# Kernel tuning notes

Measured on AMD Instinct MI355X. Metric: run time of the kernel, lower is better.

The kernel has to match this reference:

```python
import jax, jax.numpy as jnp
import numpy as np

CH = 256
RED = 4
CQK = CH // RED

def _conv(x, w, b):
    # x: [B,C,H,W], w: [O,I,3,3], b: [O]; SAME padding (pad=1)
    y = jax.lax.conv_general_dilated(
        x, w, window_strides=(1, 1), padding=((1, 1), (1, 1)),
        dimension_numbers=('NCHW', 'OIHW', 'NCHW'))
    return y + b[None, :, None, None]

def setup_inputs() -> dict:
    key = jax.random.key(0)
    ks = jax.random.split(key, 7)
    x = jax.random.normal(ks[0], (4, CH, 64, 64), dtype=jnp.float32)
    fan_in = CH * 9
    s = 1.0 / np.sqrt(fan_in)
    q_w = jax.random.uniform(ks[1], (CQK, CH, 3, 3), jnp.float32, -s, s)
    q_b = jax.random.uniform(ks[2], (CQK,), jnp.float32, -s, s)
    k_w = jax.random.uniform(ks[3], (CQK, CH, 3, 3), jnp.float32, -s, s)
    k_b = jax.random.uniform(ks[4], (CQK,), jnp.float32, -s, s)
    v_w = jax.random.uniform(ks[5], (CH, CH, 3, 3), jnp.float32, -s, s)
    v_b = jax.random.uniform(ks[6], (CH,), jnp.float32, -s, s)
    return {"x": x, "q_w": q_w, "q_b": q_b, "k_w": k_w, "k_b": k_b,
            "v_w": v_w, "v_b": v_b}

def reference(x, q_w, q_b, k_w, k_b, v_w, v_b):
    b, c, h, w = x.shape
    hw = h * w
    scale = CQK ** (-0.5)
    q = _conv(x, q_w, q_b).reshape(b, CQK, hw)   # [B, Cqk, HW]
    k = _conv(x, k_w, k_b).reshape(b, CQK, hw)   # [B, Cqk, HW]
    v = _conv(x, v_w, v_b).reshape(b, c, hw)     # [B, C,   HW]
    # attn[b,i,j] = sum_d q[b,d,i] * k[b,d,j]
    attn = jnp.einsum('bdi,bdj->bij', q, k) * scale
    attn = jax.nn.softmax(attn, axis=-1)         # [B, HW, HW]
    # out[b,c,i] = sum_j v[b,c,j] * attn[b,i,j]  (torch: bmm(v, attn^T))
    out = jnp.einsum('bcj,bij->bci', v, attn).reshape(b, c, h, w)
    return out
```

## Files before the change

### kernel.cpp

```cpp
#include <hip/hip_runtime.h>
#include <stdint.h>

typedef unsigned short u16;
typedef short short8 __attribute__((ext_vector_type(8)));
typedef short short4v __attribute__((ext_vector_type(4)));
typedef float float4v __attribute__((ext_vector_type(4)));
typedef float float16v __attribute__((ext_vector_type(16)));
typedef uint32_t uint2v __attribute__((ext_vector_type(2)));

#define HW 4096
#define QSCL 0.18033688011112042f

#define GLOAD_LDS(g, l) __builtin_amdgcn_global_load_lds( \
    (const __attribute__((address_space(1))) void*)(g),   \
    (__attribute__((address_space(3))) void*)(l), 16, 0, 0)

static __device__ __forceinline__ u16 f2bf(float f) {
  union { float f; uint32_t u; } v; v.f = f;
  uint32_t r = v.u + 0x7fffu + ((v.u >> 16) & 1u);
  return (u16)(r >> 16);
}

static __device__ __forceinline__ uint32_t pkbf(float a, float b) {
  uint32_t r;
  asm("v_cvt_pk_bf16_f32 %0, %1, %2" : "=v"(r) : "v"(a), "v"(b));
  return r;
}

__global__ __launch_bounds__(256) void k_xt(const float* __restrict__ x, u16* __restrict__ Xtp) {
  __shared__ float t[32][33];
  const int b = blockIdx.z, c0 = blockIdx.y * 32, p0 = blockIdx.x * 32;
  const int tid = threadIdx.x;
  const int l8 = tid >> 5, lp = tid & 31;
#pragma unroll
  for (int i = 0; i < 4; i++) {
    int c = l8 + i * 8;
    t[c][lp] = x[(size_t)(b * 256 + c0 + c) * HW + p0 + lp];
  }
  __syncthreads();
#pragma unroll
  for (int i = 0; i < 4; i++) {
    int p = l8 + i * 8;
    int pp = p0 + p;
    int y = pp >> 6, xx = pp & 63;
    Xtp[((size_t)(b * 66 + y + 1) * 66 + (xx + 1)) * 256 + c0 + lp] = f2bf(t[lp][p]);
  }
}

__global__ __launch_bounds__(256) void k_wprep(const float* __restrict__ qw, const float* __restrict__ qb,
    const float* __restrict__ kw, const float* __restrict__ kb,
    const float* __restrict__ vw, const float* __restrict__ vb,
    u16* __restrict__ Wt, float* __restrict__ bcat) {
  int tid = blockIdx.x * 256 + threadIdx.x;
  if (tid < 9 * 384 * 256) {
    int ci = tid & 255;
    int n = (tid >> 8) % 384;
    int off = tid / (384 * 256);
    float val;
    if (n < 64)       val = qw[(size_t)n * 2304 + ci * 9 + off];
    else if (n < 128) val = kw[(size_t)(n - 64) * 2304 + ci * 9 + off];
    else              val = vw[(size_t)(n - 128) * 2304 + ci * 9 + off];
    Wt[tid] = f2bf(val);
  }
  if (tid < 384) bcat[tid] = (tid < 64) ? qb[tid] : (tid < 128) ? kb[tid - 64] : vb[tid - 128];
}

__global__ __launch_bounds__(256) void k_conv(const u16* __restrict__ Xtp,
    const u16* __restrict__ Wt, const float* __restrict__ bcat,
    u16* __restrict__ Qt, u16* __restrict__ Kt, u16* __restrict__ Vcf) {
  __shared__ __align__(16) u16 Als[2][128 * 64];
  __shared__ __align__(16) u16 Bls[2][64 * 64];
  const int tid = threadIdx.x;
  const int b = blockIdx.z, ct = blockIdx.y;
  const int p0 = blockIdx.x * 128, n0 = ct * 64;
  const int w = tid >> 6, lane = tid & 63, l16 = lane & 15, quad = lane >> 4;

  const int lr = lane >> 3, lcx = (lane & 7) ^ lr;
  const u16* ag[4];
#pragma unroll
  for (int g = 0; g < 4; g++) {
    const int pos = p0 + w * 32 + g * 8 + lr;
    const int py = pos >> 6, px = pos & 63;
    ag[g] = Xtp + ((size_t)(b * 66 + py) * 66 + px) * 256 + lcx * 8;
  }
  const u16* bg[2];
#pragma unroll
  for (int g = 0; g < 2; g++)
    bg[g] = Wt + (size_t)(n0 + w * 16 + g * 8 + lr) * 256 + lcx * 8;

  const int rx = l16 & 7;

  float4v acc[2][4];
  const float4v zz = {0.f, 0.f, 0.f, 0.f};
#pragma unroll
  for (int i = 0; i < 2; i++)
#pragma unroll
    for (int j = 0; j < 4; j++) acc[i][j] = zz;

#pragma unroll
  for (int g = 0; g < 4; g++) GLOAD_LDS(ag[g], &Als[0][(w * 32 + g * 8) * 64]);
#pragma unroll
  for (int g = 0; g < 2; g++) GLOAD_LDS(bg[g], &Bls[0][(w * 16 + g * 8) * 64]);
  __syncthreads();

  for (int ks = 0; ks < 36; ks++) {
    const int buf = ks & 1;
    if (ks + 1 < 36) {
      const int ksn = ks + 1, tap = ksn >> 2, cg = (ksn & 3) * 64;
      const int dy = (tap * 11) >> 5, dx = tap - dy * 3;
      const int aoff = (dy * 66 + dx) * 256 + cg;
      const size_t boff = (size_t)tap * 98304 + cg;
#pragma unroll
      for (int g = 0; g < 4; g++) GLOAD_LDS(ag[g] + aoff, &Als[buf ^ 1][(w * 32 + g * 8) * 64]);
#pragma unroll
      for (int g = 0; g < 2; g++) GLOAD_LDS(bg[g] + boff, &Bls[buf ^ 1][(w * 16 + g * 8) * 64]);
    }

    short8 af[2][2], bfv[4][2];
#pragma unroll
    for (int mt = 0; mt < 2; mt++)
#pragma unroll
      for (int kk = 0; kk < 2; kk++)
        af[mt][kk] = *(const short8*)&Als[buf][(w * 32 + mt * 16 + l16) * 64 + (((kk * 4 + quad) ^ rx) * 8)];
#pragma unroll
    for (int nt = 0; nt < 4; nt++)
#pragma unroll
      for (int kk = 0; kk < 2; kk++)
        bfv[nt][kk] = *(const short8*)&Bls[buf][(nt * 16 + l16) * 64 + (((kk * 4 + quad) ^ rx) * 8)];

    if (ct < 2) {
#pragma unroll
      for (int mt = 0; mt < 2; mt++)
#pragma unroll
        for (int nt = 0; nt < 4; nt++)
#pragma unroll
          for (int kk = 0; kk < 2; kk++)
            acc[mt][nt] = __builtin_amdgcn_mfma_f32_16x16x32_bf16(bfv[nt][kk], af[mt][kk], acc[mt][nt], 0, 0, 0);
    } else {
#pragma unroll
      for (int mt = 0; mt < 2; mt++)
#pragma unroll
        for (int nt = 0; nt < 4; nt++)
#pragma unroll
          for (int kk = 0; kk < 2; kk++)
            acc[mt][nt] = __builtin_amdgcn_mfma_f32_16x16x32_bf16(af[mt][kk], bfv[nt][kk], acc[mt][nt], 0, 0, 0);
    }
    __syncthreads();
  }

  if (ct < 2) {
    u16* base = (ct == 0) ? Qt : Kt;
    const float qs = (ct == 0) ? QSCL : 1.0f;
#pragma unroll
    for (int mt = 0; mt < 2; mt++) {
      const int p = p0 + w * 32 + mt * 16 + l16;
#pragma unroll
      for (int nt = 0; nt < 4; nt++) {
        const int nb = nt * 16 + quad * 4;
        short4v o;
#pragma unroll
        for (int r = 0; r < 4; r++) o[r] = (short)f2bf((acc[mt][nt][r] + bcat[ct * 64 + nb + r]) * qs);
        *(short4v*)(base + (size_t)(b * HW + p) * 64 + nb) = o;
      }
    }
  } else {
#pragma unroll
    for (int mt = 0; mt < 2; mt++) {
      const int pb = p0 + w * 32 + mt * 16 + quad * 4;
#pragma unroll
      for (int nt = 0; nt < 4; nt++) {
        const int cl = nt * 16 + l16;
        const int gc = (ct - 2) * 64 + cl;
        const float bias = bcat[ct * 64 + cl];
        short4v o;
#pragma unroll
        for (int r = 0; r < 4; r++) o[r] = (short)f2bf(acc[mt][nt][r] + bias);
        *(short4v*)(Vcf + (size_t)(b * 256 + gc) * HW + pb) = o;
      }
    }
  }
}

__global__ __launch_bounds__(512, 2) void k_attn(const u16* __restrict__ Qt,
    const u16* __restrict__ Kt, const u16* __restrict__ Vcf, float* __restrict__ out) {
  __shared__ __align__(16) u16 Kls[2][64 * 64];
  __shared__ __align__(16) u16 Vls[2][256 * 64];
  __shared__ __align__(16) u16 Pls[64 * 64];
  __shared__ float Lls[4][64];

  const int tid = threadIdx.x;
  const int b = blockIdx.y, ib = blockIdx.x * 64;
  const int w = tid >> 6, lane = tid & 63;
  const int l16 = lane & 15, quad = lane >> 4;
  const int l32 = lane & 31, half = lane >> 5;
  const int jb = w & 3, ih = w >> 2;
  const int cb = w;

  const u16* Kb = Kt + (size_t)b * HW * 64;
  const u16* Vb = Vcf + (size_t)b * 256 * HW;

  const int lr = lane >> 3, lcx = (lane & 7) ^ lr;
  const size_t koff = (size_t)(w * 8 + lr) * 128 + (size_t)lcx * 16;
  const size_t voff = (size_t)lr * (HW * 2) + (size_t)lcx * 16;

  const int krow = (jb * 16 + l16) * 64;
  const int kc0 = (quad ^ (l16 & 7)) * 8;
  const int kc1 = ((4 + quad) ^ (l16 & 7)) * 8;

  short8 qf[2][2];
  {
    const u16* qp = Qt + ((size_t)(b * HW + ib + ih * 32 + l16)) * 64 + quad * 8;
    qf[0][0] = *(const short8*)qp;
    qf[0][1] = *(const short8*)(qp + 32);
    qf[1][0] = *(const short8*)(qp + 16 * 64);
    qf[1][1] = *(const short8*)(qp + 16 * 64 + 32);
  }

  const int vrow = (cb * 32 + l32) * 64;
  const int rx5 = l32 & 7;
  const int prow0 = l32 * 64, prow1 = (32 + l32) * 64;

  float16v of0, of1;
#pragma unroll
  for (int r = 0; r < 16; r++) { of0[r] = 0.f; of1[r] = 0.f; }
  float lp0 = 0.f, lp1 = 0.f;
  const float4v zz = {0.f, 0.f, 0.f, 0.f};

  GLOAD_LDS((const char*)Kb + koff, &Kls[0][(w * 8) * 64]);
#pragma unroll
  for (int g = 0; g < 4; g++)
    GLOAD_LDS((const char*)Vb + (size_t)(w * 32 + g * 8) * (HW * 2) + voff,
              &Vls[0][(w * 32 + g * 8) * 64]);
  __syncthreads();

  for (int jt = 0; jt < 64; jt++) {
    const int buf = jt & 1;
    {
      const int jn = ((jt + 1) & 63) * 64;
      GLOAD_LDS((const char*)Kb + (size_t)jn * 128 + koff, &Kls[buf ^ 1][(w * 8) * 64]);
#pragma unroll
      for (int g = 0; g < 4; g++)
        GLOAD_LDS((const char*)Vb + (size_t)(w * 32 + g * 8) * (HW * 2) + (size_t)jn * 2 + voff,
                  &Vls[buf ^ 1][(w * 32 + g * 8) * 64]);
    }

    short8 k0 = *(const short8*)&Kls[buf][krow + kc0];
    short8 k1 = *(const short8*)&Kls[buf][krow + kc1];
    float4v s0 = zz, s1 = zz;
    s0 = __builtin_amdgcn_mfma_f32_16x16x32_bf16(k0, qf[0][0], s0, 0, 0, 0);
    s0 = __builtin_amdgcn_mfma_f32_16x16x32_bf16(k1, qf[0][1], s0, 0, 0, 0);
    s1 = __builtin_amdgcn_mfma_f32_16x16x32_bf16(k0, qf[1][0], s1, 0, 0, 0);
    s1 = __builtin_amdgcn_mfma_f32_16x16x32_bf16(k1, qf[1][1], s1, 0, 0, 0);

    {
      float p0 = exp2f(s0[0]), p1 = exp2f(s0[1]), p2 = exp2f(s0[2]), p3 = exp2f(s0[3]);
      lp0 += (p0 + p1) + (p2 + p3);
      uint2v pd; pd[0] = pkbf(p0, p1); pd[1] = pkbf(p2, p3);
      const int row = ih * 32 + l16;
      *(uint2v*)&Pls[row * 64 + (((jb * 2 + (quad >> 1)) ^ (row & 7)) * 8) + (quad & 1) * 4] = pd;
    }
    {
      float p0 = exp2f(s1[0]), p1 = exp2f(s1[1]), p2 = exp2f(s1[2]), p3 = exp2f(s1[3]);
      lp1 += (p0 + p1) + (p2 + p3);
      uint2v pd; pd[0] = pkbf(p0, p1); pd[1] = pkbf(p2, p3);
      const int row = ih * 32 + 16 + l16;
      *(uint2v*)&Pls[row * 64 + (((jb * 2 + (quad >> 1)) ^ (row & 7)) * 8) + (quad & 1) * 4] = pd;
    }

    __builtin_amdgcn_sched_barrier(0);
    asm volatile("s_waitcnt lgkmcnt(0)" ::: "memory");
    __builtin_amdgcn_s_barrier();
    asm volatile("" ::: "memory");

    __builtin_amdgcn_s_setprio(1);
#pragma unroll
    for (int jk = 0; jk < 4; jk++) {
      const int ch = jk * 2 + half;
      short8 vf  = *(const short8*)&Vls[buf][vrow + ((ch ^ rx5) * 8)];
      short8 pf0 = *(const short8*)&Pls[prow0 + ((ch ^ rx5) * 8)];
      short8 pf1 = *(const short8*)&Pls[prow1 + ((ch ^ rx5) * 8)];
      of0 = __builtin_amdgcn_mfma_f32_32x32x16_bf16(vf, pf0, of0, 0, 0, 0);
      of1 = __builtin_amdgcn_mfma_f32_32x32x16_bf16(vf, pf1, of1, 0, 0, 0);
    }
    __builtin_amdgcn_s_setprio(0);
    __syncthreads();
  }

  lp0 += __shfl_xor(lp0, 16); lp0 += __shfl_xor(lp0, 32);
  lp1 += __shfl_xor(lp1, 16); lp1 += __shfl_xor(lp1, 32);
  if (quad == 0) {
    Lls[jb][ih * 32 + l16] = lp0;
    Lls[jb][ih * 32 + 16 + l16] = lp1;
  }
  __syncthreads();

#pragma unroll
  for (int it = 0; it < 2; it++) {
    const int ii = it * 32 + l32;
    const float inv = 1.0f / ((Lls[0][ii] + Lls[1][ii]) + (Lls[2][ii] + Lls[3][ii]));
    float* ob = out + (size_t)(b * 256 + cb * 32 + 4 * half) * HW + ib + ii;
    const float16v o = it ? of1 : of0;
#pragma unroll
    for (int r = 0; r < 16; r++)
      ob[(size_t)((r & 3) + 8 * (r >> 2)) * HW] = o[r] * inv;
  }
}

extern "C" void kernel_launch(void* const* d_in, const int* in_sizes, int n_in,
                              void* d_out, int out_size, void* d_ws, size_t ws_size,
                              hipStream_t stream) {
  const float* x  = (const float*)d_in[0];
  const float* qw = (const float*)d_in[1];
  const float* qb = (const float*)d_in[2];
  const float* kw = (const float*)d_in[3];
  const float* kb = (const float*)d_in[4];
  const float* vw = (const float*)d_in[5];
  const float* vb = (const float*)d_in[6];
  float* out = (float*)d_out;
  char* ws = (char*)d_ws;
  u16*   Xtp = (u16*)(ws);
  u16*   Wt  = (u16*)(ws + 8921088);
  float* bc  = (float*)(ws + 10690560);
  u16*   Qt  = (u16*)(ws + 10692096);
  u16*   Kt  = (u16*)(ws + 12789248);
  u16*   Vcf = (u16*)(ws + 14886400);

  hipMemsetAsync(Xtp, 0, 8921088, stream);
  k_xt  <<<dim3(128, 8, 4), 256, 0, stream>>>(x, Xtp);
  k_wprep<<<3456, 256, 0, stream>>>(qw, qb, kw, kb, vw, vb, Wt, bc);
  k_conv<<<dim3(32, 6, 4), 256, 0, stream>>>(Xtp, Wt, bc, Qt, Kt, Vcf);
  k_attn<<<dim3(64, 4), 512, 0, stream>>>(Qt, Kt, Vcf, out);
}
```

Measured before the change: 211.8 us.

## Halve attention query tile, load V directly to registers, double grid

```diff
diff --git a/kernel.cpp b/kernel.cpp
--- a/kernel.cpp
+++ b/kernel.cpp
@@ -181,129 +181,112 @@
   }
 }
 
-__global__ __launch_bounds__(512, 2) void k_attn(const u16* __restrict__ Qt,
+__global__ __launch_bounds__(512, 4) void k_attn(const u16* __restrict__ Qt,
     const u16* __restrict__ Kt, const u16* __restrict__ Vcf, float* __restrict__ out) {
   __shared__ __align__(16) u16 Kls[2][64 * 64];
-  __shared__ __align__(16) u16 Vls[2][256 * 64];
-  __shared__ __align__(16) u16 Pls[64 * 64];
-  __shared__ float Lls[4][64];
+  __shared__ __align__(16) u16 Pls[32 * 64];
+  __shared__ float Lls[4][32];
 
   const int tid = threadIdx.x;
-  const int b = blockIdx.y, ib = blockIdx.x * 64;
+  const int bid = blockIdx.x;
+  const int b = bid & 3, ib = (bid >> 2) * 32;
   const int w = tid >> 6, lane = tid & 63;
   const int l16 = lane & 15, quad = lane >> 4;
   const int l32 = lane & 31, half = lane >> 5;
   const int jb = w & 3, ih = w >> 2;
-  const int cb = w;
 
   const u16* Kb = Kt + (size_t)b * HW * 64;
-  const u16* Vb = Vcf + (size_t)b * 256 * HW;
 
   const int lr = lane >> 3, lcx = (lane & 7) ^ lr;
   const size_t koff = (size_t)(w * 8 + lr) * 128 + (size_t)lcx * 16;
-  const size_t voff = (size_t)lr * (HW * 2) + (size_t)lcx * 16;
 
   const int krow = (jb * 16 + l16) * 64;
   const int kc0 = (quad ^ (l16 & 7)) * 8;
   const int kc1 = ((4 + quad) ^ (l16 & 7)) * 8;
 
-  short8 qf[2][2];
+  const int pwo = (ih * 16 + l16) * 64 + (((jb * 2 + (quad >> 1)) ^ (l16 & 7)) * 8) + (quad & 1) * 4;
+
+  int pro[4];
+#pragma unroll
+  for (int jk = 0; jk < 4; jk++)
+    pro[jk] = l32 * 64 + (((jk * 2 + half) ^ (l32 & 7)) * 8);
+
+  const char* vp = (const char*)Vcf + ((size_t)(b * 256 + w * 32 + l32)) * (HW * 2) + half * 16;
+
+  short8 qf0, qf1;
   {
-    const u16* qp = Qt + ((size_t)(b * HW + ib + ih * 32 + l16)) * 64 + quad * 8;
-    qf[0][0] = *(const short8*)qp;
-    qf[0][1] = *(const short8*)(qp + 32);
-    qf[1][0] = *(const short8*)(qp + 16 * 64);
-    qf[1][1] = *(const short8*)(qp + 16 * 64 + 32);
-  }
-
-  const int vrow = (cb * 32 + l32) * 64;
-  const int rx5 = l32 & 7;
-  const int prow0 = l32 * 64, prow1 = (32 + l32) * 64;
-
-  float16v of0, of1;
-#pragma unroll
-  for (int r = 0; r < 16; r++) { of0[r] = 0.f; of1[r] = 0.f; }
-  float lp0 = 0.f, lp1 = 0.f;
+    const u16* qp = Qt + ((size_t)(b * HW + ib + ih * 16 + l16)) * 64 + quad * 8;
+    qf0 = *(const short8*)qp;
+    qf1 = *(const short8*)(qp + 32);
+  }
+
+  float16v of;
+#pragma unroll
+  for (int r = 0; r < 16; r++) of[r] = 0.f;
+  float lp = 0.f;
   const float4v zz = {0.f, 0.f, 0.f, 0.f};
 
   GLOAD_LDS((const char*)Kb + koff, &Kls[0][(w * 8) * 64]);
-#pragma unroll
-  for (int g = 0; g < 4; g++)
-    GLOAD_LDS((const char*)Vb + (size_t)(w * 32 + g * 8) * (HW * 2) + voff,
-              &Vls[0][(w * 32 + g * 8) * 64]);
   __syncthreads();
 
   for (int jt = 0; jt < 64; jt++) {
     const int buf = jt & 1;
+
+    short8 vf0 = *(const short8*)(vp);
+    short8 vf1 = *(const short8*)(vp + 32);
+    short8 vf2 = *(const short8*)(vp + 64);
+    short8 vf3 = *(const short8*)(vp + 96);
+
     {
       const int jn = ((jt + 1) & 63) * 64;
       GLOAD_LDS((const char*)Kb + (size_t)jn * 128 + koff, &Kls[buf ^ 1][(w * 8) * 64]);
-#pragma unroll
-      for (int g = 0; g < 4; g++)
-        GLOAD_LDS((const char*)Vb + (size_t)(w * 32 + g * 8) * (HW * 2) + (size_t)jn * 2 + voff,
-                  &Vls[buf ^ 1][(w * 32 + g * 8) * 64]);
     }
 
     short8 k0 = *(const short8*)&Kls[buf][krow + kc0];
     short8 k1 = *(const short8*)&Kls[buf][krow + kc1];
-    float4v s0 = zz, s1 = zz;
-    s0 = __builtin_amdgcn_mfma_f32_16x16x32_bf16(k0, qf[0][0], s0, 0, 0, 0);
-    s0 = __builtin_amdgcn_mfma_f32_16x16x32_bf16(k1, qf[0][1], s0, 0, 0, 0);
-    s1 = __builtin_amdgcn_mfma_f32_16x16x32_bf16(k0, qf[1][0], s1, 0, 0, 0);
-    s1 = __builtin_amdgcn_mfma_f32_16x16x32_bf16(k1, qf[1][1], s1, 0, 0, 0);
+    float4v s = zz;
+    s = __builtin_amdgcn_mfma_f32_16x16x32_bf16(k0, qf0, s, 0, 0, 0);
+    s = __builtin_amdgcn_mfma_f32_16x16x32_bf16(k1, qf1, s, 0, 0, 0);
 
     {
-      float p0 = exp2f(s0[0]), p1 = exp2f(s0[1]), p2 = exp2f(s0[2]), p3 = exp2f(s0[3]);
-      lp0 += (p0 + p1) + (p2 + p3);
+      float p0 = exp2f(s[0]), p1 = exp2f(s[1]), p2 = exp2f(s[2]), p3 = exp2f(s[3]);
+      lp += (p0 + p1) + (p2 + p3);
       uint2v pd; pd[0] = pkbf(p0, p1); pd[1] = pkbf(p2, p3);
-      const int row = ih * 32 + l16;
-      *(uint2v*)&Pls[row * 64 + (((jb * 2 + (quad >> 1)) ^ (row & 7)) * 8) + (quad & 1) * 4] = pd;
-    }
-    {
-      float p0 = exp2f(s1[0]), p1 = exp2f(s1[1]), p2 = exp2f(s1[2]), p3 = exp2f(s1[3]);
-      lp1 += (p0 + p1) + (p2 + p3);
-      uint2v pd; pd[0] = pkbf(p0, p1); pd[1] = pkbf(p2, p3);
-      const int row = ih * 32 + 16 + l16;
-      *(uint2v*)&Pls[row * 64 + (((jb * 2 + (quad >> 1)) ^ (row & 7)) * 8) + (quad & 1) * 4] = pd;
+      *(uint2v*)&Pls[pwo] = pd;
     }
 
     __builtin_amdgcn_sched_barrier(0);
     asm volatile("s_waitcnt lgkmcnt(0)" ::: "memory");
     __builtin_amdgcn_s_barrier();
-    asm volatile("" ::: "memory");
+    __builtin_amdgcn_sched_barrier(0);
 
     __builtin_amdgcn_s_setprio(1);
-#pragma unroll
-    for (int jk = 0; jk < 4; jk++) {
-      const int ch = jk * 2 + half;
-      short8 vf  = *(const short8*)&Vls[buf][vrow + ((ch ^ rx5) * 8)];
-      short8 pf0 = *(const short8*)&Pls[prow0 + ((ch ^ rx5) * 8)];
-      short8 pf1 = *(const short8*)&Pls[prow1 + ((ch ^ rx5) * 8)];
-      of0 = __builtin_amdgcn_mfma_f32_32x32x16_bf16(vf, pf0, of0, 0, 0, 0);
-      of1 = __builtin_amdgcn_mfma_f32_32x32x16_bf16(vf, pf1, of1, 0, 0, 0);
+    {
+      short8 pf0 = *(const short8*)&Pls[pro[0]];
+      of = __builtin_amdgcn_mfma_f32_32x32x16_bf16(vf0, pf0, of, 0, 0, 0);
+      short8 pf1 = *(const short8*)&Pls[pro[1]];
+      of = __builtin_amdgcn_mfma_f32_32x32x16_bf16(vf1, pf1, of, 0, 0, 0);
+      short8 pf2 = *(const short8*)&Pls[pro[2]];
+      of = __builtin_amdgcn_mfma_f32_32x32x16_bf16(vf2, pf2, of, 0, 0, 0);
+      short8 pf3 = *(const short8*)&Pls[pro[3]];
+      of = __builtin_amdgcn_mfma_f32_32x32x16_bf16(vf3, pf3, of, 0, 0, 0);
     }
     __builtin_amdgcn_s_setprio(0);
+
     __syncthreads();
-  }
-
-  lp0 += __shfl_xor(lp0, 16); lp0 += __shfl_xor(lp0, 32);
-  lp1 += __shfl_xor(lp1, 16); lp1 += __shfl_xor(lp1, 32);
-  if (quad == 0) {
-    Lls[jb][ih * 32 + l16] = lp0;
-    Lls[jb][ih * 32 + 16 + l16] = lp1;
-  }
+    vp += 128;
+  }
+
+  lp += __shfl_xor(lp, 16);
+  lp += __shfl_xor(lp, 32);
+  if (quad == 0) Lls[jb][ih * 16 + l16] = lp;
   __syncthreads();
 
-#pragma unroll
-  for (int it = 0; it < 2; it++) {
-    const int ii = it * 32 + l32;
-    const float inv = 1.0f / ((Lls[0][ii] + Lls[1][ii]) + (Lls[2][ii] + Lls[3][ii]));
-    float* ob = out + (size_t)(b * 256 + cb * 32 + 4 * half) * HW + ib + ii;
-    const float16v o = it ? of1 : of0;
-#pragma unroll
-    for (int r = 0; r < 16; r++)
-      ob[(size_t)((r & 3) + 8 * (r >> 2)) * HW] = o[r] * inv;
-  }
+  const float inv = 1.0f / ((Lls[0][l32] + Lls[1][l32]) + (Lls[2][l32] + Lls[3][l32]));
+  float* ob = out + ((size_t)(b * 256 + w * 32 + 4 * half)) * HW + ib + l32;
+#pragma unroll
+  for (int r = 0; r < 16; r++)
+    ob[(size_t)((r & 3) + 8 * (r >> 2)) * HW] = of[r] * inv;
 }
 
 extern "C" void kernel_launch(void* const* d_in, const int* in_sizes, int n_in,
@@ -329,5 +312,5 @@
   k_xt  <<<dim3(128, 8, 4), 256, 0, stream>>>(x, Xtp);
   k_wprep<<<3456, 256, 0, stream>>>(qw, qb, kw, kb, vw, vb, Wt, bc);
   k_conv<<<dim3(32, 6, 4), 256, 0, stream>>>(Xtp, Wt, bc, Qt, Kt, Vcf);
-  k_attn<<<dim3(64, 4), 512, 0, stream>>>(Qt, Kt, Vcf, out);
-}
+  k_attn<<<512, 512, 0, stream>>>(Qt, Kt, Vcf, out);
+}
```

Result: slower. 256.7 us (+21.2%).

## Triple-buffer K/V tiles, double-buffer P, one barrier per attention iteration

Applied to the files above, without the earlier changes.

```diff
diff --git a/kernel.cpp b/kernel.cpp
--- a/kernel.cpp
+++ b/kernel.cpp
@@ -183,42 +183,46 @@
 
 __global__ __launch_bounds__(512, 2) void k_attn(const u16* __restrict__ Qt,
     const u16* __restrict__ Kt, const u16* __restrict__ Vcf, float* __restrict__ out) {
-  __shared__ __align__(16) u16 Kls[2][64 * 64];
-  __shared__ __align__(16) u16 Vls[2][256 * 64];
-  __shared__ __align__(16) u16 Pls[64 * 64];
+  __shared__ __align__(16) u16 Kls[3 * 4096];
+  __shared__ __align__(16) u16 Vls[3 * 16384];
+  __shared__ __align__(16) u16 Pls[2 * 4096];
   __shared__ float Lls[4][64];
 
   const int tid = threadIdx.x;
-  const int b = blockIdx.y, ib = blockIdx.x * 64;
+  const int bid = blockIdx.x;
+  const int b = bid & 3, ib = (bid >> 2) * 64;
   const int w = tid >> 6, lane = tid & 63;
   const int l16 = lane & 15, quad = lane >> 4;
   const int l32 = lane & 31, half = lane >> 5;
   const int jb = w & 3, ih = w >> 2;
-  const int cb = w;
-
-  const u16* Kb = Kt + (size_t)b * HW * 64;
-  const u16* Vb = Vcf + (size_t)b * 256 * HW;
+
+  const char* Kb = (const char*)(Kt + (size_t)b * HW * 64);
+  const char* Vb = (const char*)(Vcf + (size_t)b * 256 * HW);
 
   const int lr = lane >> 3, lcx = (lane & 7) ^ lr;
-  const size_t koff = (size_t)(w * 8 + lr) * 128 + (size_t)lcx * 16;
-  const size_t voff = (size_t)lr * (HW * 2) + (size_t)lcx * 16;
+  const int koff = (w * 8 + lr) * 128 + lcx * 16;
+  const char* vbase = Vb + (size_t)(w * 32 + lr) * (HW * 2) + lcx * 16;
+  const int kd = w * 8 * 64;
 
   const int krow = (jb * 16 + l16) * 64;
   const int kc0 = (quad ^ (l16 & 7)) * 8;
   const int kc1 = ((4 + quad) ^ (l16 & 7)) * 8;
+
+  const int pw0 = (ih * 32 + l16) * 64 + (((jb * 2 + (quad >> 1)) ^ (l16 & 7)) * 8) + (quad & 1) * 4;
+  const int pw1 = pw0 + 16 * 64;
+
+  const int rx5 = l32 & 7;
+  const int vrow = (w * 32 + l32) * 64;
+  const int prow0 = l32 * 64, prow1 = prow0 + 32 * 64;
 
   short8 qf[2][2];
   {
     const u16* qp = Qt + ((size_t)(b * HW + ib + ih * 32 + l16)) * 64 + quad * 8;
     qf[0][0] = *(const short8*)qp;
     qf[0][1] = *(const short8*)(qp + 32);
-    qf[1][0] = *(const short8*)(qp + 16 * 64);
-    qf[1][1] = *(const short8*)(qp + 16 * 64 + 32);
-  }
-
-  const int vrow = (cb * 32 + l32) * 64;
-  const int rx5 = l32 & 7;
-  const int prow0 = l32 * 64, prow1 = (32 + l32) * 64;
+    qf[1][0] = *(const short8*)(qp + 1024);
+    qf[1][1] = *(const short8*)(qp + 1056);
+  }
 
   float16v of0, of1;
 #pragma unroll
@@ -226,26 +230,24 @@
   float lp0 = 0.f, lp1 = 0.f;
   const float4v zz = {0.f, 0.f, 0.f, 0.f};
 
-  GLOAD_LDS((const char*)Kb + koff, &Kls[0][(w * 8) * 64]);
+  GLOAD_LDS(Kb + koff, &Kls[kd]);
+  GLOAD_LDS(Kb + 8192 + koff, &Kls[4096 + kd]);
 #pragma unroll
   for (int g = 0; g < 4; g++)
-    GLOAD_LDS((const char*)Vb + (size_t)(w * 32 + g * 8) * (HW * 2) + voff,
-              &Vls[0][(w * 32 + g * 8) * 64]);
+    GLOAD_LDS(vbase + (size_t)(g * 8) * (HW * 2), &Vls[(w * 32 + g * 8) * 64]);
+#pragma unroll
+  for (int g = 0; g < 4; g++)
+    GLOAD_LDS(vbase + (size_t)(g * 8) * (HW * 2) + 128, &Vls[16384 + (w * 32 + g * 8) * 64]);
   __syncthreads();
 
+  int oKa = 0, oKb = 4096, oKc = 8192;
+  int oVa = 0, oVb = 16384, oVc = 32768;
+
   for (int jt = 0; jt < 64; jt++) {
-    const int buf = jt & 1;
-    {
-      const int jn = ((jt + 1) & 63) * 64;
-      GLOAD_LDS((const char*)Kb + (size_t)jn * 128 + koff, &Kls[buf ^ 1][(w * 8) * 64]);
-#pragma unroll
-      for (int g = 0; g < 4; g++)
-        GLOAD_LDS((const char*)Vb + (size_t)(w * 32 + g * 8) * (HW * 2) + (size_t)jn * 2 + voff,
-                  &Vls[buf ^ 1][(w * 32 + g * 8) * 64]);
-    }
-
-    short8 k0 = *(const short8*)&Kls[buf][krow + kc0];
-    short8 k1 = *(const short8*)&Kls[buf][krow + kc1];
+    const int po = (jt & 1) ? 4096 : 0;
+
+    short8 k0 = *(const short8*)&Kls[oKa + krow + kc0];
+    short8 k1 = *(const short8*)&Kls[oKa + krow + kc1];
     float4v s0 = zz, s1 = zz;
     s0 = __builtin_amdgcn_mfma_f32_16x16x32_bf16(k0, qf[0][0], s0, 0, 0, 0);
     s0 = __builtin_amdgcn_mfma_f32_16x16x32_bf16(k1, qf[0][1], s0, 0, 0, 0);
@@ -256,34 +258,39 @@
       float p0 = exp2f(s0[0]), p1 = exp2f(s0[1]), p2 = exp2f(s0[2]), p3 = exp2f(s0[3]);
       lp0 += (p0 + p1) + (p2 + p3);
       uint2v pd; pd[0] = pkbf(p0, p1); pd[1] = pkbf(p2, p3);
-      const int row = ih * 32 + l16;
-      *(uint2v*)&Pls[row * 64 + (((jb * 2 + (quad >> 1)) ^ (row & 7)) * 8) + (quad & 1) * 4] = pd;
+      *(uint2v*)&Pls[po + pw0] = pd;
     }
     {
       float p0 = exp2f(s1[0]), p1 = exp2f(s1[1]), p2 = exp2f(s1[2]), p3 = exp2f(s1[3]);
       lp1 += (p0 + p1) + (p2 + p3);
       uint2v pd; pd[0] = pkbf(p0, p1); pd[1] = pkbf(p2, p3);
-      const int row = ih * 32 + 16 + l16;
-      *(uint2v*)&Pls[row * 64 + (((jb * 2 + (quad >> 1)) ^ (row & 7)) * 8) + (quad & 1) * 4] = pd;
-    }
-
-    __builtin_amdgcn_sched_barrier(0);
-    asm volatile("s_waitcnt lgkmcnt(0)" ::: "memory");
-    __builtin_amdgcn_s_barrier();
-    asm volatile("" ::: "memory");
+      *(uint2v*)&Pls[po + pw1] = pd;
+    }
+
+    __syncthreads();
+
+    if (jt < 62) {
+      GLOAD_LDS(Kb + (size_t)(jt + 2) * 8192 + koff, &Kls[oKc + kd]);
+      const char* vt = vbase + (size_t)(jt + 2) * 128;
+#pragma unroll
+      for (int g = 0; g < 4; g++)
+        GLOAD_LDS(vt + (size_t)(g * 8) * (HW * 2), &Vls[oVc + (w * 32 + g * 8) * 64]);
+    }
 
     __builtin_amdgcn_s_setprio(1);
 #pragma unroll
     for (int jk = 0; jk < 4; jk++) {
-      const int ch = jk * 2 + half;
-      short8 vf  = *(const short8*)&Vls[buf][vrow + ((ch ^ rx5) * 8)];
-      short8 pf0 = *(const short8*)&Pls[prow0 + ((ch ^ rx5) * 8)];
-      short8 pf1 = *(const short8*)&Pls[prow1 + ((ch ^ rx5) * 8)];
+      const int co = ((jk * 2 + half) ^ rx5) * 8;
+      short8 vf  = *(const short8*)&Vls[oVa + vrow + co];
+      short8 pf0 = *(const short8*)&Pls[po + prow0 + co];
+      short8 pf1 = *(const short8*)&Pls[po + prow1 + co];
       of0 = __builtin_amdgcn_mfma_f32_32x32x16_bf16(vf, pf0, of0, 0, 0, 0);
       of1 = __builtin_amdgcn_mfma_f32_32x32x16_bf16(vf, pf1, of1, 0, 0, 0);
     }
     __builtin_amdgcn_s_setprio(0);
-    __syncthreads();
+
+    int t1 = oKa; oKa = oKb; oKb = oKc; oKc = t1;
+    int t2 = oVa; oVa = oVb; oVb = oVc; oVc = t2;
   }
 
   lp0 += __shfl_xor(lp0, 16); lp0 += __shfl_xor(lp0, 32);
@@ -298,7 +305,7 @@
   for (int it = 0; it < 2; it++) {
     const int ii = it * 32 + l32;
     const float inv = 1.0f / ((Lls[0][ii] + Lls[1][ii]) + (Lls[2][ii] + Lls[3][ii]));
-    float* ob = out + (size_t)(b * 256 + cb * 32 + 4 * half) * HW + ib + ii;
+    float* ob = out + (size_t)(b * 256 + w * 32 + 4 * half) * HW + ib + ii;
     const float16v o = it ? of1 : of0;
 #pragma unroll
     for (int r = 0; r < 16; r++)
@@ -329,5 +336,5 @@
   k_xt  <<<dim3(128, 8, 4), 256, 0, stream>>>(x, Xtp);
   k_wprep<<<3456, 256, 0, stream>>>(qw, qb, kw, kb, vw, vb, Wt, bc);
   k_conv<<<dim3(32, 6, 4), 256, 0, stream>>>(Xtp, Wt, bc, Qt, Kt, Vcf);
-  k_attn<<<dim3(64, 4), 512, 0, stream>>>(Qt, Kt, Vcf, out);
-}
+  k_attn<<<256, 512, 0, stream>>>(Qt, Kt, Vcf, out);
+}
```

After: 204.6 us. -3.4%, faster.
